# Optimization experiments

Hardware: AMD Instinct MI355X
Metric: run time of the kernel (lower is better)

## Reference

```python
import math
import jax, jax.numpy as jnp
import numpy as np

SQRT_2_OVER_PI = 0.7978845608028654
EPS = 1e-5
EPS_VAR = 1e-4
NORM_EPS = 1e-12  # F.normalize default eps


def _gelu_tanh(x):
    return 0.5 * x * (1.0 + jnp.tanh(SQRT_2_OVER_PI * (x + 0.044715 * x ** 3)))


def _normalize(v, axis):
    n = jnp.linalg.norm(v, axis=axis, keepdims=True)
    return v / jnp.maximum(n, NORM_EPS)


def setup_inputs() -> dict:
    key = jax.random.key(0)
    k_x, k_m, k_o = jax.random.split(key, 3)
    B, T, D = 8, 2048, 512
    x = jax.random.normal(k_x, (B, T, D), dtype=jnp.float32)
    ema_mean = 0.1 * jax.random.normal(k_m, (D,), dtype=jnp.float32)
    ema_sq = ema_mean ** 2 + 1.0  # ensures positive variance, like a warmed-up EMA
    ema_out = jax.random.normal(k_o, (D,), dtype=jnp.float32)
    f32 = lambda v: jnp.asarray(v, dtype=jnp.float32)
    return {
        "x": x,
        "ema_mean": ema_mean,
        "ema_sq": ema_sq,
        "ema_out": ema_out,
        "log_tau": f32(math.log(2.0)),
        "log_beta_up": f32(math.log(math.exp(0.5) - 1.0)),
        "log_beta_dn": f32(math.log(math.exp(0.5) - 1.0)),
        "log_gamma": f32(math.log(math.exp(1.0) - 1.0)),
        "log_sigma_nn": f32(math.log(math.exp(1.0) - 1.0)),
        "log_w_nn": f32(math.log(math.exp(1.0) - 1.0)),
    }


def reference(x, ema_mean, ema_sq, ema_out, log_tau, log_beta_up,
              log_beta_dn, log_gamma, log_sigma_nn, log_w_nn):
    # Steady-state (_ready=True) forward path.
    sg = jax.lax.stop_gradient
    sp = jax.nn.softplus
    tau = jnp.exp(log_tau)
    beta_up, beta_dn = sp(log_beta_up), sp(log_beta_dn)
    gamma, sigma_nn, w_nn = sp(log_gamma), sp(log_sigma_nn), sp(log_w_nn)

    out = _gelu_tanh(x)  # [B,T,D]

    # --- per-channel asymmetric EMA z-score gate (z detached) ---
    var = jnp.clip(ema_sq - ema_mean ** 2, EPS_VAR, None)  # [D]
    std = jnp.sqrt(var)
    z = sg((x - ema_mean) / (std + EPS))  # [B,T,D]
    up_arm = beta_up * jax.nn.relu(jnp.tanh(gamma * z))
    dn_arm = beta_dn * jax.nn.relu(jnp.tanh(-gamma * z))
    gate_hist = jnp.clip(1.0 + up_arm - dn_arm, 0.05, 8.0)

    # --- within-sequence nearest-neighbor novelty gate (sim detached) ---
    T = x.shape[1]
    x_n = _normalize(sg(x), axis=-1)  # [B,T,D]
    sim = jnp.einsum('btd,bsd->bts', x_n, x_n)  # [B,T,T]
    sim = jnp.where(jnp.eye(T, dtype=bool)[None], -2.0, sim)
    nn_sim = jnp.max(sim, axis=-1)  # [B,T]
    novelty_nn = (1.0 - nn_sim) * 0.5
    surp_nn = sg(jnp.tanh(sigma_nn * novelty_nn))  # sigma_nn under no_grad
    gate_nn = (1.0 + w_nn * surp_nn)[..., None]  # [B,T,1]

    # --- cosine-to-EMA-output gate (fully detached, incl. tau) ---
    out_n = _normalize(out, axis=-1)
    ema_n = _normalize(ema_out, axis=0)  # [D]
    cos_sim = jnp.clip(jnp.sum(out_n * ema_n, axis=-1), -1.0, 1.0)  # [B,T]
    gate_cos = sg(jnp.exp(-tau * cos_sim))[..., None]  # [B,T,1]

    return out * gate_hist * gate_nn * gate_cos
```

## Files before the change

kernel.cpp:

```cpp
#include <hip/hip_runtime.h>
#include <hip/hip_bf16.h>
#include <math.h>

#define BB 8
#define TT 2048
#define DD 512
#define NSL 24

typedef __attribute__((ext_vector_type(8))) short bf16x8;
typedef __attribute__((ext_vector_type(4))) float f32x4;
typedef __attribute__((ext_vector_type(4))) int i32x4;

__device__ inline float softplus_f(float v) { return log1pf(expf(v)); }

__device__ inline float tanh_fast(float y) {
    float e = __builtin_amdgcn_exp2f(y * 2.8853900817779268f);
    return 1.0f - 2.0f * __builtin_amdgcn_rcpf(e + 1.0f);
}
__device__ inline float exp_fast(float y) {
    return __builtin_amdgcn_exp2f(y * 1.4426950408889634f);
}

__device__ inline unsigned short cvt_bf16(float f) {
    __hip_bfloat16 h = (__hip_bfloat16)f;
    return *reinterpret_cast<unsigned short*>(&h);
}
__device__ inline float bf2f(unsigned short h) {
    unsigned int u = ((unsigned int)h) << 16;
    return __uint_as_float(u);
}

__device__ inline void load_lds16(const void* g, void* l) {
    __builtin_amdgcn_global_load_lds(
        (const __attribute__((address_space(1))) unsigned int*)g,
        (__attribute__((address_space(3))) unsigned int*)l, 16, 0, 0);
}

__global__ __launch_bounds__(512) void k0_prep(const float* __restrict__ ema_mean,
                                               const float* __restrict__ ema_sq,
                                               const float* __restrict__ ema_out,
                                               float* __restrict__ inv_std,
                                               float* __restrict__ ema_n) {
    __shared__ float red[8];
    int t = threadIdx.x;
    float m = ema_mean[t];
    float v = ema_sq[t] - m * m;
    v = fmaxf(v, 1e-4f);
    inv_std[t] = 1.0f / (sqrtf(v) + 1e-5f);

    float e = ema_out[t];
    float s = e * e;
#pragma unroll
    for (int off = 32; off; off >>= 1) s += __shfl_xor(s, off);
    if ((t & 63) == 0) red[t >> 6] = s;
    __syncthreads();
    if (t == 0) {
        float tot = 0.f;
        for (int i = 0; i < 8; ++i) tot += red[i];
        red[0] = 1.0f / fmaxf(sqrtf(tot), 1e-12f);
    }
    __syncthreads();
    ema_n[t] = e * red[0];
}

__global__ __launch_bounds__(256) void k1_elem(
    const float* __restrict__ x, const float* __restrict__ ema_mean,
    const float* __restrict__ inv_std, const float* __restrict__ ema_n,
    const float* __restrict__ p_log_tau, const float* __restrict__ p_lbu,
    const float* __restrict__ p_lbd, const float* __restrict__ p_lg,
    unsigned char* __restrict__ xn8, unsigned short* __restrict__ po) {
    const int row = blockIdx.x * 4 + (threadIdx.x >> 6);
    const int lane = threadIdx.x & 63;
    const size_t base = (size_t)row * DD;

    const float tau = expf(p_log_tau[0]);
    const float beta_up = softplus_f(p_lbu[0]);
    const float beta_dn = softplus_f(p_lbd[0]);
    const float gamma = softplus_f(p_lg[0]);

    float xv[8], pg[8];
    float sx2 = 0.f, so2 = 0.f, sod = 0.f;
#pragma unroll
    for (int c = 0; c < 2; ++c) {
        const int j0 = c * 256 + lane * 4;
        float4 xx = *reinterpret_cast<const float4*>(x + base + j0);
        float4 mm = *reinterpret_cast<const float4*>(ema_mean + j0);
        float4 ii = *reinterpret_cast<const float4*>(inv_std + j0);
        float4 eo = *reinterpret_cast<const float4*>(ema_n + j0);
        float vv[4] = {xx.x, xx.y, xx.z, xx.w};
        float vm[4] = {mm.x, mm.y, mm.z, mm.w};
        float vi[4] = {ii.x, ii.y, ii.z, ii.w};
        float ve[4] = {eo.x, eo.y, eo.z, eo.w};
#pragma unroll
        for (int q = 0; q < 4; ++q) {
            const int e = c * 4 + q;
            float xf = vv[q];
            xv[e] = xf;
            float x3 = xf * xf * xf;
            float gl = 0.5f * xf * (1.0f + tanh_fast(0.7978845608028654f * (xf + 0.044715f * x3)));
            float z = (xf - vm[q]) * vi[q];
            float th = tanh_fast(gamma * z);
            float up = beta_up * fmaxf(th, 0.0f);
            float dn = beta_dn * fmaxf(-th, 0.0f);
            float gh = fminf(fmaxf(1.0f + up - dn, 0.05f), 8.0f);
            pg[e] = gl * gh;
            sx2 += xf * xf;
            so2 += gl * gl;
            sod += gl * ve[q];
        }
    }
#pragma unroll
    for (int off = 32; off; off >>= 1) {
        sx2 += __shfl_xor(sx2, off);
        so2 += __shfl_xor(so2, off);
        sod += __shfl_xor(sod, off);
    }
    const float qscale = 127.0f * __builtin_amdgcn_rcpf(fmaxf(sqrtf(sx2), 1e-12f));
    float cosv = sod * __builtin_amdgcn_rcpf(fmaxf(sqrtf(so2), 1e-12f));
    cosv = fminf(fmaxf(cosv, -1.0f), 1.0f);
    const float gcos = exp_fast(-tau * cosv);

#pragma unroll
    for (int c = 0; c < 2; ++c) {
        const int j0 = c * 256 + lane * 4;
        ushort4 pb;
        pb.x = cvt_bf16(pg[c * 4 + 0] * gcos);
        pb.y = cvt_bf16(pg[c * 4 + 1] * gcos);
        pb.z = cvt_bf16(pg[c * 4 + 2] * gcos);
        pb.w = cvt_bf16(pg[c * 4 + 3] * gcos);
        *reinterpret_cast<ushort4*>(po + base + j0) = pb;
        int q0 = __float2int_rn(xv[c * 4 + 0] * qscale);
        int q1 = __float2int_rn(xv[c * 4 + 1] * qscale);
        int q2 = __float2int_rn(xv[c * 4 + 2] * qscale);
        int q3 = __float2int_rn(xv[c * 4 + 3] * qscale);
        int pk = (q0 & 255) | ((q1 & 255) << 8) | ((q2 & 255) << 16) | (q3 << 24);
        *reinterpret_cast<int*>(xn8 + base + j0) = pk;
    }
}

__global__ __launch_bounds__(512, 4) void k2_nn(const unsigned char* __restrict__ xn8,
                                                float* __restrict__ partial) {
    __shared__ char lds[73728];

    const int tid = threadIdx.x;
    const int wave = tid >> 6;
    const int lane = tid & 63;
    const int r15 = lane & 15;
    const int kgrp = lane >> 4;
    const int wr = wave >> 1;
    const int wc = wave & 1;

    const int bid = blockIdx.x;
    const int b = bid & 7;
    int t = bid >> 3;
    int tm = 0;
    while (t >= 16 - 2 * tm) { t -= 16 - 2 * tm; ++tm; }
    const int tn = 2 * tm + t;

    const size_t bbase = (size_t)b * TT * DD;
    const unsigned char* Ag = xn8 + bbase + (size_t)tm * 256 * DD;
    const unsigned char* Bg = xn8 + bbase + (size_t)tn * 128 * DD;

    i32x4 acc[4][4];
#pragma unroll
    for (int i = 0; i < 4; ++i)
#pragma unroll
        for (int j = 0; j < 4; ++j) acc[i][j] = (i32x4){0, 0, 0, 0};

    auto stage = [&](int slot, int kt) {
#pragma unroll
        for (int l = 0; l < 2; ++l) {
            const int o = l * 8192 + tid * 16;
            const int sup = o >> 7;
            const int w = (o & 127) ^ ((sup & 7) << 4);
            const int row = sup * 2 + (w >> 6);
            const int cb = w & 63;
            load_lds16(Ag + (size_t)row * DD + kt * 64 + cb, lds + slot * 24576 + o);
        }
        {
            const int o = tid * 16;
            const int sup = o >> 7;
            const int w = (o & 127) ^ ((sup & 7) << 4);
            const int row = sup * 2 + (w >> 6);
            const int cb = w & 63;
            load_lds16(Bg + (size_t)row * DD + kt * 64 + cb, lds + slot * 24576 + 16384 + o);
        }
    };

#define LADDR(R) \
    (((R) >> 1) * 128 + (((((R) & 1) << 6) + (kgrp << 4)) ^ ((((R) >> 1) & 7) << 4)))

    auto compute = [&](int slot) {
        const char* sA = lds + slot * 24576;
        const char* sB = sA + 16384;
        i32x4 av[4], bv[4];
#pragma unroll
        for (int ni = 0; ni < 4; ++ni)
            bv[ni] = *(const i32x4*)(sB + LADDR(wc * 64 + ni * 16 + r15));
#pragma unroll
        for (int mi = 0; mi < 4; ++mi)
            av[mi] = *(const i32x4*)(sA + LADDR(wr * 64 + mi * 16 + r15));
        __builtin_amdgcn_s_setprio(1);
#pragma unroll
        for (int mi = 0; mi < 4; ++mi)
#pragma unroll
            for (int ni = 0; ni < 4; ++ni)
                acc[mi][ni] = __builtin_amdgcn_mfma_i32_16x16x64_i8(av[mi], bv[ni],
                                                                    acc[mi][ni], 0, 0, 0);
        __builtin_amdgcn_s_setprio(0);
    };
#undef LADDR

    stage(0, 0);
    stage(1, 1);
    asm volatile("s_waitcnt vmcnt(3)" ::: "memory");
    __builtin_amdgcn_s_barrier();
    __builtin_amdgcn_sched_barrier(0);

#pragma unroll
    for (int kt = 0; kt < 8; ++kt) {
        if (kt + 2 < 8) stage((kt + 2) % 3, kt + 2);
        compute(kt % 3);
        if (kt < 7) {
            if (kt <= 5)
                asm volatile("s_waitcnt vmcnt(3)" ::: "memory");
            else
                asm volatile("s_waitcnt vmcnt(0)" ::: "memory");
            __builtin_amdgcn_s_barrier();
            __builtin_amdgcn_sched_barrier(0);
        }
    }

    const float inv_qq = 1.0f / (127.0f * 127.0f);
    const int doff = 128 * (tn - 2 * tm);
    const bool isdiag = (doff == 0) || (doff == 128);
    float accf[4][4][4];
#pragma unroll
    for (int mi = 0; mi < 4; ++mi)
#pragma unroll
        for (int ni = 0; ni < 4; ++ni)
#pragma unroll
            for (int rr = 0; rr < 4; ++rr) {
                float e = (float)acc[mi][ni][rr] * inv_qq;
                if (isdiag) {
                    const int rl = wr * 64 + mi * 16 + kgrp * 4 + rr;
                    const int cl = wc * 64 + ni * 16 + r15;
                    if (rl == cl + doff) e = -2.0f;
                }
                accf[mi][ni][rr] = e;
            }
    float rmx[4][4];
#pragma unroll
    for (int mi = 0; mi < 4; ++mi)
#pragma unroll
        for (int rr = 0; rr < 4; ++rr) {
            float v = fmaxf(fmaxf(accf[mi][0][rr], accf[mi][1][rr]),
                            fmaxf(accf[mi][2][rr], accf[mi][3][rr]));
            v = fmaxf(v, __shfl_xor(v, 1));
            v = fmaxf(v, __shfl_xor(v, 2));
            v = fmaxf(v, __shfl_xor(v, 4));
            v = fmaxf(v, __shfl_xor(v, 8));
            rmx[mi][rr] = v;
        }
    float cmx[4];
#pragma unroll
    for (int ni = 0; ni < 4; ++ni) {
        float v = -2.0f;
#pragma unroll
        for (int mi = 0; mi < 4; ++mi)
#pragma unroll
            for (int rr = 0; rr < 4; ++rr) v = fmaxf(v, accf[mi][ni][rr]);
        v = fmaxf(v, __shfl_xor(v, 16));
        v = fmaxf(v, __shfl_xor(v, 32));
        cmx[ni] = v;
    }
    __syncthreads();
    float* rbuf = (float*)lds;
    float* cbuf = (float*)(lds + 2048);
    if (r15 == 0) {
#pragma unroll
        for (int mi = 0; mi < 4; ++mi)
#pragma unroll
            for (int rr = 0; rr < 4; ++rr)
                rbuf[(wr * 64 + mi * 16 + kgrp * 4 + rr) * 2 + wc] = rmx[mi][rr];
    }
    if (kgrp == 0) {
#pragma unroll
        for (int ni = 0; ni < 4; ++ni)
            cbuf[(wc * 64 + ni * 16 + r15) * 4 + wr] = cmx[ni];
    }
    __syncthreads();
    if (tid < 256) {
        const float v = fmaxf(rbuf[tid * 2 + 0], rbuf[tid * 2 + 1]);
        partial[((size_t)b * TT + tm * 256 + tid) * NSL + tn] = v;
    } else if (tid < 384) {
        const int c = tid - 256;
        const float v = fmaxf(fmaxf(cbuf[c * 4 + 0], cbuf[c * 4 + 1]),
                              fmaxf(cbuf[c * 4 + 2], cbuf[c * 4 + 3]));
        partial[((size_t)b * TT + tn * 128 + c) * NSL + 16 + tm] = v;
    }
}

__global__ __launch_bounds__(256) void k3_scale(float* __restrict__ out,
                                                const unsigned short* __restrict__ po,
                                                const float* __restrict__ partial,
                                                const float* __restrict__ p_lsn,
                                                const float* __restrict__ p_lwn) {
    const int row = blockIdx.x * 4 + (threadIdx.x >> 6);
    const int lane = threadIdx.x & 63;
    const float sigma_nn = softplus_f(p_lsn[0]);
    const float w_nn = softplus_f(p_lwn[0]);

    const int rb = row & (TT - 1);
    const int tmr = rb >> 8;
    const int tnr = rb >> 7;
    const int idx = lane & 31;
    float v = -2.0f;
    if (idx < 16) {
        if (idx >= 2 * tmr) v = partial[(size_t)row * NSL + idx];
    } else if (idx < NSL) {
        if (idx - 16 <= (tnr >> 1)) v = partial[(size_t)row * NSL + idx];
    }
    v = fmaxf(v, __shfl_xor(v, 1));
    v = fmaxf(v, __shfl_xor(v, 2));
    v = fmaxf(v, __shfl_xor(v, 4));
    v = fmaxf(v, __shfl_xor(v, 8));
    v = fmaxf(v, __shfl_xor(v, 16));
    const float g = 1.0f + w_nn * tanh_fast(sigma_nn * 0.5f * (1.0f - v));

    const size_t base = (size_t)row * DD + lane * 8;
    ushort4 p0 = *reinterpret_cast<const ushort4*>(po + base);
    ushort4 p1 = *reinterpret_cast<const ushort4*>(po + base + 4);
    float4 o0, o1;
    o0.x = bf2f(p0.x) * g; o0.y = bf2f(p0.y) * g;
    o0.z = bf2f(p0.z) * g; o0.w = bf2f(p0.w) * g;
    o1.x = bf2f(p1.x) * g; o1.y = bf2f(p1.y) * g;
    o1.z = bf2f(p1.z) * g; o1.w = bf2f(p1.w) * g;
    *reinterpret_cast<float4*>(out + base) = o0;
    *reinterpret_cast<float4*>(out + base + 4) = o1;
}

extern "C" void kernel_launch(void* const* d_in, const int* in_sizes, int n_in,
                              void* d_out, int out_size, void* d_ws, size_t ws_size,
                              hipStream_t stream) {
    const float* x = (const float*)d_in[0];
    const float* ema_mean = (const float*)d_in[1];
    const float* ema_sq = (const float*)d_in[2];
    const float* ema_out = (const float*)d_in[3];
    const float* log_tau = (const float*)d_in[4];
    const float* log_beta_up = (const float*)d_in[5];
    const float* log_beta_dn = (const float*)d_in[6];
    const float* log_gamma = (const float*)d_in[7];
    const float* log_sigma_nn = (const float*)d_in[8];
    const float* log_w_nn = (const float*)d_in[9];

    char* ws = (char*)d_ws;
    unsigned char* XN8 = (unsigned char*)ws;
    unsigned short* PO = (unsigned short*)(ws + 8388608);
    float* partial = (float*)(ws + 8388608 + 16777216);
    float* inv_std = (float*)(ws + 8388608 + 16777216 + 1572864);
    float* ema_n = (float*)(ws + 8388608 + 16777216 + 1572864 + 2048);
    float* out = (float*)d_out;

    hipLaunchKernelGGL(k0_prep, dim3(1), dim3(512), 0, stream, ema_mean, ema_sq, ema_out,
                       inv_std, ema_n);
    hipLaunchKernelGGL(k1_elem, dim3(BB * TT / 4), dim3(256), 0, stream, x, ema_mean, inv_std,
                       ema_n, log_tau, log_beta_up, log_beta_dn, log_gamma, XN8, PO);
    hipLaunchKernelGGL(k2_nn, dim3(BB * 72), dim3(512), 0, stream, XN8, partial);
    hipLaunchKernelGGL(k3_scale, dim3(BB * TT / 4), dim3(256), 0, stream, out, PO, partial,
                       log_sigma_nn, log_w_nn);
}
```

Before: 61.64 us.

## Shrink NN-gemm tiles to 128x128 and fold prep kernel into elementwise pass

The prep kernel is removed: inverse std and the EMA output norm are now recomputed inside the elementwise kernel, which saves one launch. The int8 similarity kernel moves from 256x128 tiles with 512 threads and a 3-stage manual pipeline to 128x128 symmetric tiles with 256 threads and a 2-stage double buffer. This raises the block count from 576 to 1088 and uses less LDS per block. The partial-max layout widens to 32 slots, so the final reduction gains one extra shuffle step. The trade is simpler synchronisation and more blocks, at the cost of less operand reuse per block and a less deeply overlapped load pipeline.

Result: no change. 60.72 us (-1.5%).

```diff
diff --git a/kernel.cpp b/kernel.cpp
--- a/kernel.cpp
+++ b/kernel.cpp
@@ -5,7 +5,7 @@
 #define BB 8
 #define TT 2048
 #define DD 512
-#define NSL 24
+#define NSL 32
 
 typedef __attribute__((ext_vector_type(8))) short bf16x8;
 typedef __attribute__((ext_vector_type(4))) float f32x4;
@@ -36,36 +36,9 @@
         (__attribute__((address_space(3))) unsigned int*)l, 16, 0, 0);
 }
 
-__global__ __launch_bounds__(512) void k0_prep(const float* __restrict__ ema_mean,
-                                               const float* __restrict__ ema_sq,
-                                               const float* __restrict__ ema_out,
-                                               float* __restrict__ inv_std,
-                                               float* __restrict__ ema_n) {
-    __shared__ float red[8];
-    int t = threadIdx.x;
-    float m = ema_mean[t];
-    float v = ema_sq[t] - m * m;
-    v = fmaxf(v, 1e-4f);
-    inv_std[t] = 1.0f / (sqrtf(v) + 1e-5f);
-
-    float e = ema_out[t];
-    float s = e * e;
-#pragma unroll
-    for (int off = 32; off; off >>= 1) s += __shfl_xor(s, off);
-    if ((t & 63) == 0) red[t >> 6] = s;
-    __syncthreads();
-    if (t == 0) {
-        float tot = 0.f;
-        for (int i = 0; i < 8; ++i) tot += red[i];
-        red[0] = 1.0f / fmaxf(sqrtf(tot), 1e-12f);
-    }
-    __syncthreads();
-    ema_n[t] = e * red[0];
-}
-
 __global__ __launch_bounds__(256) void k1_elem(
     const float* __restrict__ x, const float* __restrict__ ema_mean,
-    const float* __restrict__ inv_std, const float* __restrict__ ema_n,
+    const float* __restrict__ ema_sq, const float* __restrict__ ema_out,
     const float* __restrict__ p_log_tau, const float* __restrict__ p_lbu,
     const float* __restrict__ p_lbd, const float* __restrict__ p_lg,
     unsigned char* __restrict__ xn8, unsigned short* __restrict__ po) {
@@ -79,17 +52,17 @@
     const float gamma = softplus_f(p_lg[0]);
 
     float xv[8], pg[8];
-    float sx2 = 0.f, so2 = 0.f, sod = 0.f;
+    float sx2 = 0.f, so2 = 0.f, sod = 0.f, se2 = 0.f;
 #pragma unroll
     for (int c = 0; c < 2; ++c) {
         const int j0 = c * 256 + lane * 4;
         float4 xx = *reinterpret_cast<const float4*>(x + base + j0);
         float4 mm = *reinterpret_cast<const float4*>(ema_mean + j0);
-        float4 ii = *reinterpret_cast<const float4*>(inv_std + j0);
-        float4 eo = *reinterpret_cast<const float4*>(ema_n + j0);
+        float4 qq = *reinterpret_cast<const float4*>(ema_sq + j0);
+        float4 eo = *reinterpret_cast<const float4*>(ema_out + j0);
         float vv[4] = {xx.x, xx.y, xx.z, xx.w};
         float vm[4] = {mm.x, mm.y, mm.z, mm.w};
-        float vi[4] = {ii.x, ii.y, ii.z, ii.w};
+        float vq[4] = {qq.x, qq.y, qq.z, qq.w};
         float ve[4] = {eo.x, eo.y, eo.z, eo.w};
 #pragma unroll
         for (int q = 0; q < 4; ++q) {
@@ -98,7 +71,9 @@
             xv[e] = xf;
             float x3 = xf * xf * xf;
             float gl = 0.5f * xf * (1.0f + tanh_fast(0.7978845608028654f * (xf + 0.044715f * x3)));
-            float z = (xf - vm[q]) * vi[q];
+            float var = fmaxf(vq[q] - vm[q] * vm[q], 1e-4f);
+            float istd = __builtin_amdgcn_rcpf(sqrtf(var) + 1e-5f);
+            float z = (xf - vm[q]) * istd;
             float th = tanh_fast(gamma * z);
             float up = beta_up * fmaxf(th, 0.0f);
             float dn = beta_dn * fmaxf(-th, 0.0f);
@@ -107,6 +82,7 @@
             sx2 += xf * xf;
             so2 += gl * gl;
             sod += gl * ve[q];
+            se2 += ve[q] * ve[q];
         }
     }
 #pragma unroll
@@ -114,9 +90,11 @@
         sx2 += __shfl_xor(sx2, off);
         so2 += __shfl_xor(so2, off);
         sod += __shfl_xor(sod, off);
+        se2 += __shfl_xor(se2, off);
     }
     const float qscale = 127.0f * __builtin_amdgcn_rcpf(fmaxf(sqrtf(sx2), 1e-12f));
-    float cosv = sod * __builtin_amdgcn_rcpf(fmaxf(sqrtf(so2), 1e-12f));
+    const float inv_en = __builtin_amdgcn_rcpf(fmaxf(sqrtf(se2), 1e-12f));
+    float cosv = sod * inv_en * __builtin_amdgcn_rcpf(fmaxf(sqrtf(so2), 1e-12f));
     cosv = fminf(fmaxf(cosv, -1.0f), 1.0f);
     const float gcos = exp_fast(-tau * cosv);
 
@@ -138,9 +116,9 @@
     }
 }
 
-__global__ __launch_bounds__(512, 4) void k2_nn(const unsigned char* __restrict__ xn8,
+__global__ __launch_bounds__(256, 4) void k2_nn(const unsigned char* __restrict__ xn8,
                                                 float* __restrict__ partial) {
-    __shared__ char lds[73728];
+    __shared__ char lds[32768];
 
     const int tid = threadIdx.x;
     const int wave = tid >> 6;
@@ -154,11 +132,11 @@
     const int b = bid & 7;
     int t = bid >> 3;
     int tm = 0;
-    while (t >= 16 - 2 * tm) { t -= 16 - 2 * tm; ++tm; }
-    const int tn = 2 * tm + t;
+    while (t >= 16 - tm) { t -= 16 - tm; ++tm; }
+    const int tn = tm + t;
 
     const size_t bbase = (size_t)b * TT * DD;
-    const unsigned char* Ag = xn8 + bbase + (size_t)tm * 256 * DD;
+    const unsigned char* Ag = xn8 + bbase + (size_t)tm * 128 * DD;
     const unsigned char* Bg = xn8 + bbase + (size_t)tn * 128 * DD;
 
     i32x4 acc[4][4];
@@ -170,20 +148,13 @@
     auto stage = [&](int slot, int kt) {
 #pragma unroll
         for (int l = 0; l < 2; ++l) {
-            const int o = l * 8192 + tid * 16;
+            const int o = l * 4096 + tid * 16;
             const int sup = o >> 7;
             const int w = (o & 127) ^ ((sup & 7) << 4);
             const int row = sup * 2 + (w >> 6);
             const int cb = w & 63;
-            load_lds16(Ag + (size_t)row * DD + kt * 64 + cb, lds + slot * 24576 + o);
-        }
-        {
-            const int o = tid * 16;
-            const int sup = o >> 7;
-            const int w = (o & 127) ^ ((sup & 7) << 4);
-            const int row = sup * 2 + (w >> 6);
-            const int cb = w & 63;
-            load_lds16(Bg + (size_t)row * DD + kt * 64 + cb, lds + slot * 24576 + 16384 + o);
+            load_lds16(Ag + (size_t)row * DD + kt * 64 + cb, lds + slot * 16384 + o);
+            load_lds16(Bg + (size_t)row * DD + kt * 64 + cb, lds + slot * 16384 + 8192 + o);
         }
     };
 
@@ -191,8 +162,8 @@
     (((R) >> 1) * 128 + (((((R) & 1) << 6) + (kgrp << 4)) ^ ((((R) >> 1) & 7) << 4)))
 
     auto compute = [&](int slot) {
-        const char* sA = lds + slot * 24576;
-        const char* sB = sA + 16384;
+        const char* sA = lds + slot * 16384;
+        const char* sB = sA + 8192;
         i32x4 av[4], bv[4];
 #pragma unroll
         for (int ni = 0; ni < 4; ++ni)
@@ -212,28 +183,16 @@
 #undef LADDR
 
     stage(0, 0);
-    stage(1, 1);
-    asm volatile("s_waitcnt vmcnt(3)" ::: "memory");
-    __builtin_amdgcn_s_barrier();
-    __builtin_amdgcn_sched_barrier(0);
-
+    __syncthreads();
 #pragma unroll
     for (int kt = 0; kt < 8; ++kt) {
-        if (kt + 2 < 8) stage((kt + 2) % 3, kt + 2);
-        compute(kt % 3);
-        if (kt < 7) {
-            if (kt <= 5)
-                asm volatile("s_waitcnt vmcnt(3)" ::: "memory");
-            else
-                asm volatile("s_waitcnt vmcnt(0)" ::: "memory");
-            __builtin_amdgcn_s_barrier();
-            __builtin_amdgcn_sched_barrier(0);
-        }
+        if (kt < 7) stage((kt + 1) & 1, kt + 1);
+        compute(kt & 1);
+        if (kt < 7) __syncthreads();
     }
 
     const float inv_qq = 1.0f / (127.0f * 127.0f);
-    const int doff = 128 * (tn - 2 * tm);
-    const bool isdiag = (doff == 0) || (doff == 128);
+    const bool diag = (tm == tn);
     float accf[4][4][4];
 #pragma unroll
     for (int mi = 0; mi < 4; ++mi)
@@ -242,10 +201,10 @@
 #pragma unroll
             for (int rr = 0; rr < 4; ++rr) {
                 float e = (float)acc[mi][ni][rr] * inv_qq;
-                if (isdiag) {
+                if (diag) {
                     const int rl = wr * 64 + mi * 16 + kgrp * 4 + rr;
                     const int cl = wc * 64 + ni * 16 + r15;
-                    if (rl == cl + doff) e = -2.0f;
+                    if (rl == cl) e = -2.0f;
                 }
                 accf[mi][ni][rr] = e;
             }
@@ -276,7 +235,7 @@
     }
     __syncthreads();
     float* rbuf = (float*)lds;
-    float* cbuf = (float*)(lds + 2048);
+    float* cbuf = (float*)(lds + 1024);
     if (r15 == 0) {
 #pragma unroll
         for (int mi = 0; mi < 4; ++mi)
@@ -287,16 +246,15 @@
     if (kgrp == 0) {
 #pragma unroll
         for (int ni = 0; ni < 4; ++ni)
-            cbuf[(wc * 64 + ni * 16 + r15) * 4 + wr] = cmx[ni];
+            cbuf[(wc * 64 + ni * 16 + r15) * 2 + wr] = cmx[ni];
     }
     __syncthreads();
-    if (tid < 256) {
+    if (tid < 128) {
         const float v = fmaxf(rbuf[tid * 2 + 0], rbuf[tid * 2 + 1]);
-        partial[((size_t)b * TT + tm * 256 + tid) * NSL + tn] = v;
-    } else if (tid < 384) {
-        const int c = tid - 256;
-        const float v = fmaxf(fmaxf(cbuf[c * 4 + 0], cbuf[c * 4 + 1]),
-                              fmaxf(cbuf[c * 4 + 2], cbuf[c * 4 + 3]));
+        partial[((size_t)b * TT + tm * 128 + tid) * NSL + tn] = v;
+    } else if (!diag) {
+        const int c = tid - 128;
+        const float v = fmaxf(cbuf[c * 2 + 0], cbuf[c * 2 + 1]);
         partial[((size_t)b * TT + tn * 128 + c) * NSL + 16 + tm] = v;
     }
 }
@@ -311,21 +269,19 @@
     const float sigma_nn = softplus_f(p_lsn[0]);
     const float w_nn = softplus_f(p_lwn[0]);
 
-    const int rb = row & (TT - 1);
-    const int tmr = rb >> 8;
-    const int tnr = rb >> 7;
-    const int idx = lane & 31;
+    const int p = (row & (TT - 1)) >> 7;
     float v = -2.0f;
-    if (idx < 16) {
-        if (idx >= 2 * tmr) v = partial[(size_t)row * NSL + idx];
-    } else if (idx < NSL) {
-        if (idx - 16 <= (tnr >> 1)) v = partial[(size_t)row * NSL + idx];
+    if (lane < 16) {
+        if (lane >= p) v = partial[(size_t)row * NSL + lane];
+    } else if (lane < NSL) {
+        if (lane - 16 < p) v = partial[(size_t)row * NSL + lane];
     }
     v = fmaxf(v, __shfl_xor(v, 1));
     v = fmaxf(v, __shfl_xor(v, 2));
     v = fmaxf(v, __shfl_xor(v, 4));
     v = fmaxf(v, __shfl_xor(v, 8));
     v = fmaxf(v, __shfl_xor(v, 16));
+    v = fmaxf(v, __shfl_xor(v, 32));
     const float g = 1.0f + w_nn * tanh_fast(sigma_nn * 0.5f * (1.0f - v));
 
     const size_t base = (size_t)row * DD + lane * 8;
@@ -358,15 +314,11 @@
     unsigned char* XN8 = (unsigned char*)ws;
     unsigned short* PO = (unsigned short*)(ws + 8388608);
     float* partial = (float*)(ws + 8388608 + 16777216);
-    float* inv_std = (float*)(ws + 8388608 + 16777216 + 1572864);
-    float* ema_n = (float*)(ws + 8388608 + 16777216 + 1572864 + 2048);
     float* out = (float*)d_out;
 
-    hipLaunchKernelGGL(k0_prep, dim3(1), dim3(512), 0, stream, ema_mean, ema_sq, ema_out,
-                       inv_std, ema_n);
-    hipLaunchKernelGGL(k1_elem, dim3(BB * TT / 4), dim3(256), 0, stream, x, ema_mean, inv_std,
-                       ema_n, log_tau, log_beta_up, log_beta_dn, log_gamma, XN8, PO);
-    hipLaunchKernelGGL(k2_nn, dim3(BB * 72), dim3(512), 0, stream, XN8, partial);
+    hipLaunchKernelGGL(k1_elem, dim3(BB * TT / 4), dim3(256), 0, stream, x, ema_mean, ema_sq,
+                       ema_out, log_tau, log_beta_up, log_beta_dn, log_gamma, XN8, PO);
+    hipLaunchKernelGGL(k2_nn, dim3(BB * 136), dim3(256), 0, stream, XN8, partial);
     hipLaunchKernelGGL(k3_scale, dim3(BB * TT / 4), dim3(256), 0, stream, out, PO, partial,
                        log_sigma_nn, log_w_nn);
 }
```
